# Optimization experiments

Measured on AMD Instinct MI355X. Metric: run time of the kernel, lower is better.

Reference implementation:

```python
import jax, jax.numpy as jnp
import numpy as np

N_NODES = 100000
N_EDGES = 1600000
IN_CH = 64
OUT_CH = 32
HEADS = 4
NEG_SLOPE = 0.2


def setup_inputs() -> dict:
    key = jax.random.key(0)
    k = jax.random.split(key, 6)
    x = jax.random.normal(k[0], (N_NODES, IN_CH), dtype=jnp.float32)
    edge_index = jax.random.randint(k[1], (2, N_EDGES), 0, N_NODES, dtype=jnp.int32)
    W = jax.random.normal(k[2], (IN_CH, HEADS * OUT_CH), dtype=jnp.float32) * 0.1
    att_src = jax.random.normal(k[3], (1, HEADS, OUT_CH), dtype=jnp.float32) * 0.1
    att_dst = jax.random.normal(k[4], (1, HEADS, OUT_CH), dtype=jnp.float32) * 0.1
    bias = jnp.zeros((HEADS * OUT_CH,), dtype=jnp.float32)
    return {"x": x, "edge_index": edge_index, "W": W,
            "att_src": att_src, "att_dst": att_dst, "bias": bias}


def reference(x, edge_index, W, att_src, att_dst, bias):
    N = x.shape[0]
    H, C = att_src.shape[1], att_src.shape[2]
    # GATConv defaults: add self loops
    loop = jnp.arange(N, dtype=edge_index.dtype)
    src = jnp.concatenate([edge_index[0], loop])  # [E+N]
    dst = jnp.concatenate([edge_index[1], loop])  # [E+N]
    # linear transform -> [N, H, C]
    h = (x @ W).reshape(N, H, C)
    # per-node attention halves: [N, H]
    a_src = jnp.sum(h * att_src, axis=-1)
    a_dst = jnp.sum(h * att_dst, axis=-1)
    # edge scores with LeakyReLU: [E+N, H]
    e = jax.nn.leaky_relu(a_src[src] + a_dst[dst], negative_slope=NEG_SLOPE)
    # segment softmax over destination nodes (numerically stable)
    m = jax.ops.segment_max(e, dst, num_segments=N)           # [N, H]
    m = jnp.where(jnp.isfinite(m), m, 0.0)
    ex = jnp.exp(e - m[dst])                                   # [E+N, H]
    denom = jax.ops.segment_sum(ex, dst, num_segments=N)      # [N, H]
    alpha = ex / (denom[dst] + 1e-16)                          # [E+N, H]
    # scatter-aggregate weighted source features -> [N, H, C]
    out = jax.ops.segment_sum(h[src] * alpha[:, :, None], dst, num_segments=N)
    out = out.reshape(N, H * C) + bias
    return jax.nn.log_softmax(out, axis=1)
```

## Files before the change

### kernel.cpp

```cpp
#include <hip/hip_runtime.h>
#include <hip/hip_bf16.h>

#define IN_CH 64
#define HC 128
#define NHEAD 4
#define NEG 0.2f
#define CAPB 32
#define BWID 128
#define NB 782
#define CAP2 2560
#define CH1 4096
#define VPT 8

typedef short s16x8 __attribute__((ext_vector_type(8)));
typedef float f32x4 __attribute__((ext_vector_type(4)));

__device__ __forceinline__ float leaky(float v) { return fmaxf(v, NEG * v); }
__device__ __forceinline__ unsigned short f2bf(float f) {
    unsigned int u = __float_as_uint(f);
    u += 0x7fff + ((u >> 16) & 1);
    return (unsigned short)(u >> 16);
}
__device__ __forceinline__ float4 add4(float4 a, float4 b) {
    return make_float4(a.x + b.x, a.y + b.y, a.z + b.z, a.w + b.w);
}
__device__ __forceinline__ float4 leaky4(float4 v) {
    return make_float4(leaky(v.x), leaky(v.y), leaky(v.z), leaky(v.w));
}
__device__ __forceinline__ float4 exp4(float4 v) {
    return make_float4(__expf(v.x), __expf(v.y), __expf(v.z), __expf(v.w));
}
__device__ __forceinline__ float comp4(float4 v, int i) {
    float r = v.x;
    r = (i == 1) ? v.y : r;
    r = (i == 2) ? v.z : r;
    r = (i == 3) ? v.w : r;
    return r;
}

#define ACC8(al, hv)                                                  \
    do {                                                              \
        acc[0] = fmaf((al), __uint_as_float((hv).x << 16), acc[0]);   \
        acc[1] = fmaf((al), __uint_as_float((hv).x & 0xffff0000u), acc[1]); \
        acc[2] = fmaf((al), __uint_as_float((hv).y << 16), acc[2]);   \
        acc[3] = fmaf((al), __uint_as_float((hv).y & 0xffff0000u), acc[3]); \
        acc[4] = fmaf((al), __uint_as_float((hv).z << 16), acc[4]);   \
        acc[5] = fmaf((al), __uint_as_float((hv).z & 0xffff0000u), acc[5]); \
        acc[6] = fmaf((al), __uint_as_float((hv).w << 16), acc[6]);   \
        acc[7] = fmaf((al), __uint_as_float((hv).w & 0xffff0000u), acc[7]); \
    } while (0)

__global__ void __launch_bounds__(256) k_prep(
        const float* __restrict__ W, const float* __restrict__ att_src,
        const float* __restrict__ att_dst, unsigned short* __restrict__ wtp,
        int* __restrict__ bcnt) {
    const int t = threadIdx.x;
    for (int i = t; i < NB * 16; i += 256) bcnt[i] = 0;
    for (int idx = t; idx < 144 * 64; idx += 256) {
        const int c = idx >> 6, k = idx & 63;
        float v = 0.f;
        if (c < HC) v = W[k * HC + c];
        else if (c < HC + 8) {
            const int j = c - HC, h = j & 3;
            const float* att = (j < 4) ? att_src : att_dst;
#pragma unroll
            for (int cc = 0; cc < 32; ++cc)
                v += W[k * HC + h * 32 + cc] * att[h * 32 + cc];
        }
        wtp[c * 72 + k] = f2bf(v);
    }
    for (int idx = t; idx < 144 * 8; idx += 256)
        wtp[(idx >> 3) * 72 + 64 + (idx & 7)] = 0;
}

__global__ void __launch_bounds__(512, 2) k_xform(
        const float* __restrict__ x, const unsigned short* __restrict__ wtp,
        unsigned short* __restrict__ h_bf, float* __restrict__ a_src,
        float* __restrict__ a_dst, int N) {
    __shared__ unsigned short xs[128][72];
    __shared__ unsigned short wt[144][72];
    const int t = threadIdx.x;
    const int rowbase_blk = blockIdx.x * 128;

    for (int idx = t; idx < 1296; idx += 512)
        ((uint4*)wt)[idx] = ((const uint4*)wtp)[idx];
    for (int idx = t; idx < (128 * IN_CH) / 4; idx += 512) {
        const int row = idx >> 4;
        const int c0 = (idx & 15) * 4;
        const int grow = min(rowbase_blk + row, N - 1);
        const float4 v = ((const float4*)(x + (size_t)grow * IN_CH))[idx & 15];
        const unsigned int p0 = (unsigned int)f2bf(v.x) | ((unsigned int)f2bf(v.y) << 16);
        const unsigned int p1 = (unsigned int)f2bf(v.z) | ((unsigned int)f2bf(v.w) << 16);
        *(uint2*)&xs[row][c0] = make_uint2(p0, p1);
    }
    __syncthreads();

    const int lane = t & 63;
    const int w = t >> 6;
    const int rbase = w * 16;
    const int lr = lane & 15, lq = lane >> 4;

    f32x4 acc[9];
#pragma unroll
    for (int n = 0; n < 9; ++n) acc[n] = (f32x4){0.f, 0.f, 0.f, 0.f};

#pragma unroll
    for (int ks = 0; ks < 2; ++ks) {
        const s16x8 xb = *(const s16x8*)&xs[rbase + lr][ks * 32 + lq * 8];
#pragma unroll
        for (int n = 0; n < 9; ++n) {
            const s16x8 wa = *(const s16x8*)&wt[n * 16 + lr][ks * 32 + lq * 8];
            acc[n] = __builtin_amdgcn_mfma_f32_16x16x32_bf16(wa, xb, acc[n], 0, 0, 0);
        }
    }

    const int node = rowbase_blk + rbase + lr;
    if (node < N) {
#pragma unroll
        for (int n = 0; n < 8; ++n) {
            const unsigned int p0 = (unsigned int)f2bf(acc[n][0]) |
                                    ((unsigned int)f2bf(acc[n][1]) << 16);
            const unsigned int p1 = (unsigned int)f2bf(acc[n][2]) |
                                    ((unsigned int)f2bf(acc[n][3]) << 16);
            *(uint2*)(h_bf + (size_t)node * HC + n * 16 + lq * 4) = make_uint2(p0, p1);
        }
        if (lq == 0)
            *(float4*)(a_src + node * NHEAD) =
                make_float4(acc[8][0], acc[8][1], acc[8][2], acc[8][3]);
        else if (lq == 1)
            *(float4*)(a_dst + node * NHEAD) =
                make_float4(acc[8][0], acc[8][1], acc[8][2], acc[8][3]);
    }
}

__global__ void __launch_bounds__(512, 2) k_bin(
        const int* __restrict__ src, const int* __restrict__ dst,
        int* __restrict__ bcnt, int* __restrict__ pairs, int E) {
    __shared__ int hist[NB];
    __shared__ int scanbuf[1024];
    __shared__ int startb[NB];
    __shared__ int gbase[NB];
    __shared__ int lbuf[CH1];
    __shared__ int gposb[CH1];
    const int t = threadIdx.x;
    const int base = blockIdx.x * CH1;
    const int cnt = min(CH1, E - base);

    for (int i = t; i < NB; i += 512) hist[i] = 0;
    __syncthreads();

    int pk[VPT]; int rb[VPT];
#pragma unroll
    for (int k = 0; k < VPT; ++k) {
        const int idx = base + k * 512 + t;
        if (idx < E) {
            const int s = src[idx], d = dst[idx];
            const int b = d >> 7;
            const int dl = d & 127;
            pk[k] = (dl << 17) | s;
            const int rank = atomicAdd(&hist[b], 1);
            rb[k] = (b << 16) | rank;
        } else {
            pk[k] = 0; rb[k] = -1;
        }
    }
    __syncthreads();

    scanbuf[t] = (t < NB) ? hist[t] : 0;
    scanbuf[t + 512] = (t + 512 < NB) ? hist[t + 512] : 0;
    __syncthreads();
    for (int off = 1; off < 1024; off <<= 1) {
        const int a0 = (t >= off) ? scanbuf[t - off] : 0;
        const int a1 = (t + 512 >= off) ? scanbuf[t + 512 - off] : 0;
        __syncthreads();
        scanbuf[t] += a0;
        scanbuf[t + 512] += a1;
        __syncthreads();
    }
    for (int i = t; i < NB; i += 512) {
        const int h = hist[i];
        startb[i] = scanbuf[i] - h;
        gbase[i] = (h > 0) ? atomicAdd(&bcnt[i * 16], h) : 0;
    }
    __syncthreads();

#pragma unroll
    for (int k = 0; k < VPT; ++k) {
        if (rb[k] >= 0) {
            const int b = rb[k] >> 16;
            const int rank = rb[k] & 0xffff;
            const int lpos = startb[b] + rank;
            const int gp = gbase[b] + rank;
            lbuf[lpos] = pk[k];
            gposb[lpos] = (gp < CAP2) ? (b * CAP2 + gp) : -1;
        }
    }
    __syncthreads();

    for (int i = t; i < cnt; i += 512) {
        const int g = gposb[i];
        if (g >= 0) pairs[g] = lbuf[i];
    }
}

__global__ void __launch_bounds__(256) k_fill(
        const int* __restrict__ bcnt, const int* __restrict__ pairs,
        int* __restrict__ srcbuf, int* __restrict__ rowstart,
        int* __restrict__ deg, int N) {
    const int b = blockIdx.x;
    const int t = threadIdx.x;
    __shared__ int scnt[BWID];
    __shared__ int cur[BWID];
    __shared__ int scan2[256];
    __shared__ int slist[CAP2];
    __shared__ int sbase_s;

    int part = 0;
    for (int i = t; i < b; i += 256) part += min(bcnt[i * 16], CAP2);
    scan2[t] = part; __syncthreads();
    for (int off = 128; off > 0; off >>= 1) {
        if (t < off) scan2[t] += scan2[t + off];
        __syncthreads();
    }
    if (t == 0) sbase_s = scan2[0];
    if (t < BWID) scnt[t] = 0;
    __syncthreads();

    const int mc = min(bcnt[b * 16], CAP2);
    const int pb = b * CAP2;

    for (int i = t; i < mc; i += 256)
        atomicAdd(&scnt[pairs[pb + i] >> 17], 1);
    __syncthreads();

    if (t < BWID) scan2[t] = scnt[t];
    __syncthreads();
    for (int off = 1; off < BWID; off <<= 1) {
        const int add = (t >= off && t < BWID) ? scan2[t - off] : 0;
        __syncthreads();
        if (t < BWID) scan2[t] += add;
        __syncthreads();
    }
    if (t < BWID) {
        const int ex = scan2[t] - scnt[t];
        cur[t] = ex;
        const int n = b * BWID + t;
        if (n < N) {
            rowstart[n] = sbase_s + ex;
            deg[n] = scnt[t];
        }
    }
    __syncthreads();

    for (int i = t; i < mc; i += 256) {
        const int e = pairs[pb + i];
        const int p = atomicAdd(&cur[e >> 17], 1);
        slist[p] = e & 0x1ffff;
    }
    __syncthreads();

    for (int i = t; i < mc; i += 256) srcbuf[sbase_s + i] = slist[i];
}

__global__ void __launch_bounds__(256) k_node(
        const int* __restrict__ deg_, const int* __restrict__ rowstart,
        const int* __restrict__ srcbuf,
        const float* __restrict__ a_src, const float* __restrict__ a_dst,
        const unsigned short* __restrict__ h_bf, const float* __restrict__ bias,
        float* __restrict__ out, int N) {
    const int slot = threadIdx.x >> 4;
    const int l = threadIdx.x & 15;
    int n = blockIdx.x * 16 + slot;
    n = min(n, N - 1);
    const int deg = deg_[n];
    const int start = rowstart[n];
    const int dcap = min(deg, CAPB);

    __shared__ float s_ex[16][CAPB + 1][NHEAD];
    __shared__ int   s_src[16][CAPB + 1];

    const float4 ad4  = *(const float4*)(a_dst + n * NHEAD);
    const float4 asn4 = *(const float4*)(a_src + n * NHEAD);

    float4 sum4 = make_float4(0.f, 0.f, 0.f, 0.f);
    for (int j = l; j < dcap; j += 16) {
        const int s = srcbuf[start + j];
        s_src[slot][j] = s;
        const float4 a = *(const float4*)(a_src + s * NHEAD);
        const float4 e4 = exp4(leaky4(add4(a, ad4)));
        *(float4*)&s_ex[slot][j][0] = e4;
        sum4 = add4(sum4, e4);
    }
    for (int j = CAPB + l; j < deg; j += 16) {
        const int s = srcbuf[start + j];
        const float4 a = *(const float4*)(a_src + s * NHEAD);
        sum4 = add4(sum4, exp4(leaky4(add4(a, ad4))));
    }
#pragma unroll
    for (int off = 1; off < 16; off <<= 1) {
        sum4.x += __shfl_xor(sum4.x, off, 64);
        sum4.y += __shfl_xor(sum4.y, off, 64);
        sum4.z += __shfl_xor(sum4.z, off, 64);
        sum4.w += __shfl_xor(sum4.w, off, 64);
    }
    const float4 self4 = exp4(leaky4(add4(asn4, ad4)));
    sum4 = add4(sum4, self4);
    const float4 r4v = make_float4(1.f / (sum4.x + 1e-16f), 1.f / (sum4.y + 1e-16f),
                                   1.f / (sum4.z + 1e-16f), 1.f / (sum4.w + 1e-16f));

    __builtin_amdgcn_wave_barrier();

    const int hd = l >> 2;
    const float rsel = comp4(r4v, hd);
    const float adh  = comp4(ad4, hd);
    float acc[8];
#pragma unroll
    for (int k = 0; k < 8; ++k) acc[k] = 0.f;

    int j = 0;
    for (; j + 2 <= dcap; j += 2) {
        const int s0 = s_src[slot][j];
        const int s1 = s_src[slot][j + 1];
        const uint4 h0 = *(const uint4*)(h_bf + (size_t)s0 * HC + l * 8);
        const uint4 h1 = *(const uint4*)(h_bf + (size_t)s1 * HC + l * 8);
        const float al0 = s_ex[slot][j][hd];
        const float al1 = s_ex[slot][j + 1][hd];
        ACC8(al0, h0);
        ACC8(al1, h1);
    }
    if (j < dcap) {
        const int s0 = s_src[slot][j];
        const uint4 h0 = *(const uint4*)(h_bf + (size_t)s0 * HC + l * 8);
        const float al0 = s_ex[slot][j][hd];
        ACC8(al0, h0);
    }
    for (int jj = CAPB; jj < deg; ++jj) {
        const int s = srcbuf[start + jj];
        const float al = __expf(leaky(a_src[s * NHEAD + hd] + adh));
        const uint4 hv = *(const uint4*)(h_bf + (size_t)s * HC + l * 8);
        ACC8(al, hv);
    }
    {
        const float als = comp4(self4, hd);
        const uint4 hv = *(const uint4*)(h_bf + (size_t)n * HC + l * 8);
        ACC8(als, hv);
    }

    const float4 b0 = *(const float4*)(bias + l * 8);
    const float4 b1 = *(const float4*)(bias + l * 8 + 4);
    acc[0] = acc[0] * rsel + b0.x; acc[1] = acc[1] * rsel + b0.y;
    acc[2] = acc[2] * rsel + b0.z; acc[3] = acc[3] * rsel + b0.w;
    acc[4] = acc[4] * rsel + b1.x; acc[5] = acc[5] * rsel + b1.y;
    acc[6] = acc[6] * rsel + b1.z; acc[7] = acc[7] * rsel + b1.w;

    float mxv = fmaxf(fmaxf(fmaxf(acc[0], acc[1]), fmaxf(acc[2], acc[3])),
                      fmaxf(fmaxf(acc[4], acc[5]), fmaxf(acc[6], acc[7])));
#pragma unroll
    for (int off = 1; off < 16; off <<= 1) mxv = fmaxf(mxv, __shfl_xor(mxv, off, 64));
    float se = 0.f;
#pragma unroll
    for (int k = 0; k < 8; ++k) se += __expf(acc[k] - mxv);
#pragma unroll
    for (int off = 1; off < 16; off <<= 1) se += __shfl_xor(se, off, 64);
    const float lse = mxv + __logf(se);

    float* op = out + (size_t)n * HC + l * 8;
    *(float4*)op = make_float4(acc[0] - lse, acc[1] - lse, acc[2] - lse, acc[3] - lse);
    *(float4*)(op + 4) = make_float4(acc[4] - lse, acc[5] - lse, acc[6] - lse, acc[7] - lse);
}

extern "C" void kernel_launch(void* const* d_in, const int* in_sizes, int n_in,
                              void* d_out, int out_size, void* d_ws, size_t ws_size,
                              hipStream_t stream) {
    const float* x       = (const float*)d_in[0];
    const int*   ei      = (const int*)d_in[1];
    const float* W       = (const float*)d_in[2];
    const float* att_src = (const float*)d_in[3];
    const float* att_dst = (const float*)d_in[4];
    const float* bias    = (const float*)d_in[5];
    float* out = (float*)d_out;

    const int N = in_sizes[0] / IN_CH;
    const int E = in_sizes[1] / 2;
    const int* src = ei;
    const int* dst = ei + E;

    char* wsb = (char*)d_ws;
    unsigned short* h_bf = (unsigned short*)wsb;    wsb += (size_t)N * HC * 2;
    float* a_src  = (float*)wsb;                    wsb += (size_t)N * NHEAD * 4;
    float* a_dst  = (float*)wsb;                    wsb += (size_t)N * NHEAD * 4;
    int*   bcnt   = (int*)wsb;                      wsb += (size_t)NB * 16 * 4;
    int*   pairs  = (int*)wsb;                      wsb += (size_t)NB * CAP2 * 4;
    int*   srcbuf = (int*)wsb;                      wsb += (size_t)E * 4;
    int*   rowstart = (int*)wsb;                    wsb += (size_t)N * 4;
    int*   deg    = (int*)wsb;                      wsb += (size_t)N * 4;
    unsigned short* wtp = (unsigned short*)wsb;     wsb += 144 * 72 * 2;

    const int NXB = (N + 127) / 128;
    const int NBB = (E + CH1 - 1) / CH1;

    k_prep<<<1, 256, 0, stream>>>(W, att_src, att_dst, wtp, bcnt);
    k_xform<<<NXB, 512, 0, stream>>>(x, wtp, h_bf, a_src, a_dst, N);
    k_bin<<<NBB, 512, 0, stream>>>(src, dst, bcnt, pairs, E);
    k_fill<<<NB, 256, 0, stream>>>(bcnt, pairs, srcbuf, rowstart, deg, N);
    k_node<<<(N + 15) / 16, 256, 0, stream>>>(deg, rowstart, srcbuf,
                                              a_src, a_dst,
                                              (const unsigned short*)h_bf, bias, out, N);
}
```

Measured before the change: 224.6 us.

## Fuse node transform and CSR fill into one interleaved kernel

Removes the separate weight-prep and transform kernels and merges the node transform with the per-bin CSR fill into one launch. Even blocks do the MFMA transform and odd blocks do the fill, using a shared-memory union. Each transform block now rebuilds the bf16 weight tile from W itself, and bcnt is cleared with a memset. The fill writes srcbuf at a fixed per-bin offset (b*CAP2) instead of a prefix sum over earlier bins, so the scan and its serial dependency go away at the cost of a padded srcbuf. This cuts launch count and lets compute-heavy and memory-heavy blocks overlap, but redundant weight conversion in every transform block adds some work.

After: 235.0 us. 4.6% more time.

```diff
diff --git a/kernel.cpp b/kernel.cpp
--- a/kernel.cpp
+++ b/kernel.cpp
@@ -49,89 +49,6 @@
         acc[6] = fmaf((al), __uint_as_float((hv).w << 16), acc[6]);   \
         acc[7] = fmaf((al), __uint_as_float((hv).w & 0xffff0000u), acc[7]); \
     } while (0)
-
-__global__ void __launch_bounds__(256) k_prep(
-        const float* __restrict__ W, const float* __restrict__ att_src,
-        const float* __restrict__ att_dst, unsigned short* __restrict__ wtp,
-        int* __restrict__ bcnt) {
-    const int t = threadIdx.x;
-    for (int i = t; i < NB * 16; i += 256) bcnt[i] = 0;
-    for (int idx = t; idx < 144 * 64; idx += 256) {
-        const int c = idx >> 6, k = idx & 63;
-        float v = 0.f;
-        if (c < HC) v = W[k * HC + c];
-        else if (c < HC + 8) {
-            const int j = c - HC, h = j & 3;
-            const float* att = (j < 4) ? att_src : att_dst;
-#pragma unroll
-            for (int cc = 0; cc < 32; ++cc)
-                v += W[k * HC + h * 32 + cc] * att[h * 32 + cc];
-        }
-        wtp[c * 72 + k] = f2bf(v);
-    }
-    for (int idx = t; idx < 144 * 8; idx += 256)
-        wtp[(idx >> 3) * 72 + 64 + (idx & 7)] = 0;
-}
-
-__global__ void __launch_bounds__(512, 2) k_xform(
-        const float* __restrict__ x, const unsigned short* __restrict__ wtp,
-        unsigned short* __restrict__ h_bf, float* __restrict__ a_src,
-        float* __restrict__ a_dst, int N) {
-    __shared__ unsigned short xs[128][72];
-    __shared__ unsigned short wt[144][72];
-    const int t = threadIdx.x;
-    const int rowbase_blk = blockIdx.x * 128;
-
-    for (int idx = t; idx < 1296; idx += 512)
-        ((uint4*)wt)[idx] = ((const uint4*)wtp)[idx];
-    for (int idx = t; idx < (128 * IN_CH) / 4; idx += 512) {
-        const int row = idx >> 4;
-        const int c0 = (idx & 15) * 4;
-        const int grow = min(rowbase_blk + row, N - 1);
-        const float4 v = ((const float4*)(x + (size_t)grow * IN_CH))[idx & 15];
-        const unsigned int p0 = (unsigned int)f2bf(v.x) | ((unsigned int)f2bf(v.y) << 16);
-        const unsigned int p1 = (unsigned int)f2bf(v.z) | ((unsigned int)f2bf(v.w) << 16);
-        *(uint2*)&xs[row][c0] = make_uint2(p0, p1);
-    }
-    __syncthreads();
-
-    const int lane = t & 63;
-    const int w = t >> 6;
-    const int rbase = w * 16;
-    const int lr = lane & 15, lq = lane >> 4;
-
-    f32x4 acc[9];
-#pragma unroll
-    for (int n = 0; n < 9; ++n) acc[n] = (f32x4){0.f, 0.f, 0.f, 0.f};
-
-#pragma unroll
-    for (int ks = 0; ks < 2; ++ks) {
-        const s16x8 xb = *(const s16x8*)&xs[rbase + lr][ks * 32 + lq * 8];
-#pragma unroll
-        for (int n = 0; n < 9; ++n) {
-            const s16x8 wa = *(const s16x8*)&wt[n * 16 + lr][ks * 32 + lq * 8];
-            acc[n] = __builtin_amdgcn_mfma_f32_16x16x32_bf16(wa, xb, acc[n], 0, 0, 0);
-        }
-    }
-
-    const int node = rowbase_blk + rbase + lr;
-    if (node < N) {
-#pragma unroll
-        for (int n = 0; n < 8; ++n) {
-            const unsigned int p0 = (unsigned int)f2bf(acc[n][0]) |
-                                    ((unsigned int)f2bf(acc[n][1]) << 16);
-            const unsigned int p1 = (unsigned int)f2bf(acc[n][2]) |
-                                    ((unsigned int)f2bf(acc[n][3]) << 16);
-            *(uint2*)(h_bf + (size_t)node * HC + n * 16 + lq * 4) = make_uint2(p0, p1);
-        }
-        if (lq == 0)
-            *(float4*)(a_src + node * NHEAD) =
-                make_float4(acc[8][0], acc[8][1], acc[8][2], acc[8][3]);
-        else if (lq == 1)
-            *(float4*)(a_dst + node * NHEAD) =
-                make_float4(acc[8][0], acc[8][1], acc[8][2], acc[8][3]);
-    }
-}
 
 __global__ void __launch_bounds__(512, 2) k_bin(
         const int* __restrict__ src, const int* __restrict__ dst,
@@ -203,63 +120,128 @@
     }
 }
 
-__global__ void __launch_bounds__(256) k_fill(
+__global__ void __launch_bounds__(512, 2) k_mid(
+        const float* __restrict__ x, const float* __restrict__ W,
+        const float* __restrict__ att_src, const float* __restrict__ att_dst,
+        unsigned short* __restrict__ h_bf, float* __restrict__ a_src,
+        float* __restrict__ a_dst,
         const int* __restrict__ bcnt, const int* __restrict__ pairs,
         int* __restrict__ srcbuf, int* __restrict__ rowstart,
         int* __restrict__ deg, int N) {
-    const int b = blockIdx.x;
+    __shared__ union {
+        struct { unsigned short xs[128][72]; unsigned short wt[144][72]; } xf;
+        struct { int slist[CAP2]; int scnt[BWID]; int cur[BWID]; int scan2[BWID]; } fl;
+    } sm;
     const int t = threadIdx.x;
-    __shared__ int scnt[BWID];
-    __shared__ int cur[BWID];
-    __shared__ int scan2[256];
-    __shared__ int slist[CAP2];
-    __shared__ int sbase_s;
-
-    int part = 0;
-    for (int i = t; i < b; i += 256) part += min(bcnt[i * 16], CAP2);
-    scan2[t] = part; __syncthreads();
-    for (int off = 128; off > 0; off >>= 1) {
-        if (t < off) scan2[t] += scan2[t + off];
-        __syncthreads();
-    }
-    if (t == 0) sbase_s = scan2[0];
-    if (t < BWID) scnt[t] = 0;
-    __syncthreads();
-
-    const int mc = min(bcnt[b * 16], CAP2);
-    const int pb = b * CAP2;
-
-    for (int i = t; i < mc; i += 256)
-        atomicAdd(&scnt[pairs[pb + i] >> 17], 1);
-    __syncthreads();
-
-    if (t < BWID) scan2[t] = scnt[t];
-    __syncthreads();
-    for (int off = 1; off < BWID; off <<= 1) {
-        const int add = (t >= off && t < BWID) ? scan2[t - off] : 0;
-        __syncthreads();
-        if (t < BWID) scan2[t] += add;
-        __syncthreads();
-    }
-    if (t < BWID) {
-        const int ex = scan2[t] - scnt[t];
-        cur[t] = ex;
-        const int n = b * BWID + t;
-        if (n < N) {
-            rowstart[n] = sbase_s + ex;
-            deg[n] = scnt[t];
-        }
-    }
-    __syncthreads();
-
-    for (int i = t; i < mc; i += 256) {
-        const int e = pairs[pb + i];
-        const int p = atomicAdd(&cur[e >> 17], 1);
-        slist[p] = e & 0x1ffff;
-    }
-    __syncthreads();
-
-    for (int i = t; i < mc; i += 256) srcbuf[sbase_s + i] = slist[i];
+
+    if ((blockIdx.x & 1) == 0) {
+        const int xb = blockIdx.x >> 1;
+        const int rowbase_blk = xb * 128;
+
+        for (int idx = t; idx < (IN_CH * HC) / 4; idx += 512) {
+            const float4 v = ((const float4*)W)[idx];
+            const int k = idx >> 5;
+            const int c0 = (idx & 31) * 4;
+            sm.xf.wt[c0 + 0][k] = f2bf(v.x);
+            sm.xf.wt[c0 + 1][k] = f2bf(v.y);
+            sm.xf.wt[c0 + 2][k] = f2bf(v.z);
+            sm.xf.wt[c0 + 3][k] = f2bf(v.w);
+        }
+        for (int idx = t; idx < 16 * 64; idx += 512) {
+            const int j = idx >> 6, k = idx & 63;
+            float v = 0.f;
+            if (j < 8) {
+                const int h = j & 3;
+                const float* att = (j < 4) ? att_src : att_dst;
+#pragma unroll
+                for (int c = 0; c < 32; ++c)
+                    v += W[k * HC + h * 32 + c] * att[h * 32 + c];
+            }
+            sm.xf.wt[128 + j][k] = f2bf(v);
+        }
+        for (int idx = t; idx < (128 * IN_CH) / 4; idx += 512) {
+            const int row = idx >> 4;
+            const int c0 = (idx & 15) * 4;
+            const int grow = min(rowbase_blk + row, N - 1);
+            const float4 v = ((const float4*)(x + (size_t)grow * IN_CH))[idx & 15];
+            const unsigned int p0 = (unsigned int)f2bf(v.x) | ((unsigned int)f2bf(v.y) << 16);
+            const unsigned int p1 = (unsigned int)f2bf(v.z) | ((unsigned int)f2bf(v.w) << 16);
+            *(uint2*)&sm.xf.xs[row][c0] = make_uint2(p0, p1);
+        }
+        __syncthreads();
+
+        const int lane = t & 63;
+        const int w = t >> 6;
+        const int rbase = w * 16;
+        const int lr = lane & 15, lq = lane >> 4;
+
+        f32x4 acc[9];
+#pragma unroll
+        for (int n = 0; n < 9; ++n) acc[n] = (f32x4){0.f, 0.f, 0.f, 0.f};
+
+#pragma unroll
+        for (int ks = 0; ks < 2; ++ks) {
+            const s16x8 xbf = *(const s16x8*)&sm.xf.xs[rbase + lr][ks * 32 + lq * 8];
+#pragma unroll
+            for (int n = 0; n < 9; ++n) {
+                const s16x8 wa = *(const s16x8*)&sm.xf.wt[n * 16 + lr][ks * 32 + lq * 8];
+                acc[n] = __builtin_amdgcn_mfma_f32_16x16x32_bf16(wa, xbf, acc[n], 0, 0, 0);
+            }
+        }
+
+        const int node = rowbase_blk + rbase + lr;
+        if (node < N) {
+#pragma unroll
+            for (int n = 0; n < 8; ++n) {
+                const unsigned int p0 = (unsigned int)f2bf(acc[n][0]) |
+                                        ((unsigned int)f2bf(acc[n][1]) << 16);
+                const unsigned int p1 = (unsigned int)f2bf(acc[n][2]) |
+                                        ((unsigned int)f2bf(acc[n][3]) << 16);
+                *(uint2*)(h_bf + (size_t)node * HC + n * 16 + lq * 4) = make_uint2(p0, p1);
+            }
+            if (lq == 0)
+                *(float4*)(a_src + node * NHEAD) =
+                    make_float4(acc[8][0], acc[8][1], acc[8][2], acc[8][3]);
+            else if (lq == 1)
+                *(float4*)(a_dst + node * NHEAD) =
+                    make_float4(acc[8][0], acc[8][1], acc[8][2], acc[8][3]);
+        }
+    } else {
+        const int b = blockIdx.x >> 1;
+        const int mc = min(bcnt[b * 16], CAP2);
+        const int pb = b * CAP2;
+
+        if (t < BWID) sm.fl.scnt[t] = 0;
+        __syncthreads();
+        for (int i = t; i < mc; i += 512)
+            atomicAdd(&sm.fl.scnt[pairs[pb + i] >> 17], 1);
+        __syncthreads();
+        if (t < BWID) sm.fl.scan2[t] = sm.fl.scnt[t];
+        __syncthreads();
+        for (int off = 1; off < BWID; off <<= 1) {
+            const int add = (t < BWID && t >= off) ? sm.fl.scan2[t - off] : 0;
+            __syncthreads();
+            if (t < BWID) sm.fl.scan2[t] += add;
+            __syncthreads();
+        }
+        if (t < BWID) {
+            const int ex = sm.fl.scan2[t] - sm.fl.scnt[t];
+            sm.fl.cur[t] = ex;
+            const int n = b * BWID + t;
+            if (n < N) {
+                rowstart[n] = pb + ex;
+                deg[n] = sm.fl.scnt[t];
+            }
+        }
+        __syncthreads();
+        for (int i = t; i < mc; i += 512) {
+            const int e = pairs[pb + i];
+            const int p = atomicAdd(&sm.fl.cur[e >> 17], 1);
+            sm.fl.slist[p] = e & 0x1ffff;
+        }
+        __syncthreads();
+        for (int i = t; i < mc; i += 512) srcbuf[pb + i] = sm.fl.slist[i];
+    }
 }
 
 __global__ void __launch_bounds__(256) k_node(
@@ -391,18 +373,18 @@
     float* a_dst  = (float*)wsb;                    wsb += (size_t)N * NHEAD * 4;
     int*   bcnt   = (int*)wsb;                      wsb += (size_t)NB * 16 * 4;
     int*   pairs  = (int*)wsb;                      wsb += (size_t)NB * CAP2 * 4;
-    int*   srcbuf = (int*)wsb;                      wsb += (size_t)E * 4;
+    int*   srcbuf = (int*)wsb;                      wsb += (size_t)NB * CAP2 * 4;
     int*   rowstart = (int*)wsb;                    wsb += (size_t)N * 4;
     int*   deg    = (int*)wsb;                      wsb += (size_t)N * 4;
-    unsigned short* wtp = (unsigned short*)wsb;     wsb += 144 * 72 * 2;
-
-    const int NXB = (N + 127) / 128;
+
     const int NBB = (E + CH1 - 1) / CH1;
 
-    k_prep<<<1, 256, 0, stream>>>(W, att_src, att_dst, wtp, bcnt);
-    k_xform<<<NXB, 512, 0, stream>>>(x, wtp, h_bf, a_src, a_dst, N);
+    hipMemsetAsync(bcnt, 0, (size_t)NB * 16 * 4, stream);
+
     k_bin<<<NBB, 512, 0, stream>>>(src, dst, bcnt, pairs, E);
-    k_fill<<<NB, 256, 0, stream>>>(bcnt, pairs, srcbuf, rowstart, deg, N);
+    k_mid<<<NB * 2, 512, 0, stream>>>(x, W, att_src, att_dst,
+                                      h_bf, a_src, a_dst,
+                                      bcnt, pairs, srcbuf, rowstart, deg, N);
     k_node<<<(N + 15) / 16, 256, 0, stream>>>(deg, rowstart, srcbuf,
                                               a_src, a_dst,
                                               (const unsigned short*)h_bf, bias, out, N);
```
